# Performance work log

Measured on AMD Instinct MI355X. Metric: run time of the kernel, lower is better.

Reference implementation:

```python
import jax, jax.numpy as jnp
import numpy as np

N_HEAD, D_MODEL, D_K, D_V = 8, 512, 64, 64
B, S = 4, 2048
LN_EPS = 1e-5


def setup_inputs() -> dict:
    key = jax.random.key(0)
    ks = jax.random.split(key, 12)
    std_qk = np.sqrt(2.0 / (D_MODEL + D_K))
    std_v = np.sqrt(2.0 / (D_MODEL + D_V))
    return {
        "q": jax.random.normal(ks[0], (B, S, D_MODEL), jnp.float32),
        "k": jax.random.normal(ks[1], (B, S, D_MODEL), jnp.float32),
        "v": jax.random.normal(ks[2], (B, S, D_MODEL), jnp.float32),
        "w_qs": jax.random.normal(ks[3], (N_HEAD * D_K, D_MODEL), jnp.float32) * std_qk,
        "b_qs": jnp.zeros((N_HEAD * D_K,), jnp.float32),
        "w_ks": jax.random.normal(ks[4], (N_HEAD * D_K, D_MODEL), jnp.float32) * std_qk,
        "b_ks": jnp.zeros((N_HEAD * D_K,), jnp.float32),
        "w_vs": jax.random.normal(ks[5], (N_HEAD * D_V, D_MODEL), jnp.float32) * std_v,
        "b_vs": jnp.zeros((N_HEAD * D_V,), jnp.float32),
        "w_fc": jax.random.normal(ks[6], (D_MODEL, N_HEAD * D_V), jnp.float32) * np.sqrt(2.0 / (D_MODEL + N_HEAD * D_V)),
        "b_fc": jnp.zeros((D_MODEL,), jnp.float32),
        "ln_g": jnp.ones((D_MODEL,), jnp.float32),
        "ln_b": jnp.zeros((D_MODEL,), jnp.float32),
    }


def reference(q, k, v, w_qs, b_qs, w_ks, b_ks, w_vs, b_vs, w_fc, b_fc, ln_g, ln_b):
    sz_b, len_q, _ = q.shape
    residual = q
    temperature = np.power(D_K, 0.5).astype(np.float32)
    # Projections: [b, s, h*dk] -> [h, b, s, dk]  (matches permute(2,0,1,3))
    qh = (jnp.einsum('bsd,fd->bsf', q, w_qs) + b_qs).reshape(sz_b, len_q, N_HEAD, D_K).transpose(2, 0, 1, 3)
    kh = (jnp.einsum('bsd,fd->bsf', k, w_ks) + b_ks).reshape(sz_b, -1, N_HEAD, D_K).transpose(2, 0, 1, 3)
    vh = (jnp.einsum('bsd,fd->bsf', v, w_vs) + b_vs).reshape(sz_b, -1, N_HEAD, D_V).transpose(2, 0, 1, 3)
    # Scaled dot-product attention (dropout is identity in eval)
    attn = jnp.einsum('hbqd,hbkd->hbqk', qh, kh) / temperature
    attn = jax.nn.softmax(attn, axis=-1)
    out = jnp.einsum('hbqk,hbkv->hbqv', attn, vh)          # [h, b, q, dv]
    out = out.transpose(1, 2, 0, 3).reshape(sz_b, len_q, N_HEAD * D_V)
    out = jnp.einsum('bsf,df->bsd', out, w_fc) + b_fc
    # Residual + LayerNorm
    x = out + residual
    mu = jnp.mean(x, axis=-1, keepdims=True)
    var = jnp.mean(jnp.square(x - mu), axis=-1, keepdims=True)
    x = (x - mu) * jax.lax.rsqrt(var + LN_EPS) * ln_g + ln_b
    # attn returned as [(n_head*b), len_q, len_k] to match torch bmm layout
    return x, attn.reshape(N_HEAD * sz_b, len_q, -1)
```

## Files before the change

kernel.cpp:

```cpp
#include <hip/hip_runtime.h>
#include <hip/hip_bf16.h>

constexpr int NB  = 4;
constexpr int NS  = 2048;
constexpr int NH  = 8;
constexpr int DM  = 512;
constexpr int DKV = 64;
constexpr int HB  = NH * NB;

typedef __attribute__((ext_vector_type(8))) short short8;
typedef __attribute__((ext_vector_type(4))) float f32x4;

__device__ inline unsigned short f2bf(float f) {
    unsigned u = __builtin_bit_cast(unsigned, f);
    u = (u + 0x7fffu + ((u >> 16) & 1u)) >> 16;
    return (unsigned short)u;
}
__device__ inline float bf2f(unsigned short h) {
    unsigned u = ((unsigned)h) << 16;
    return __builtin_bit_cast(float, u);
}
__device__ inline short8 ld8(const unsigned short* p) { return *(const short8*)p; }

__device__ inline short8 pack8(const float* p) {
    f32x4 a = *(const f32x4*)p;
    f32x4 b = *(const f32x4*)(p + 4);
    short8 r;
    r[0] = (short)f2bf(a[0]); r[1] = (short)f2bf(a[1]);
    r[2] = (short)f2bf(a[2]); r[3] = (short)f2bf(a[3]);
    r[4] = (short)f2bf(b[0]); r[5] = (short)f2bf(b[1]);
    r[6] = (short)f2bf(b[2]); r[7] = (short)f2bf(b[3]);
    return r;
}

__device__ inline f32x4 mfma16(short8 a, short8 b, f32x4 c) {
    return __builtin_amdgcn_mfma_f32_16x16x32_bf16(a, b, c, 0, 0, 0);
}

__device__ inline void gl_lds16(const void* g, void* l) {
    __builtin_amdgcn_global_load_lds(
        (const __attribute__((address_space(1))) unsigned*)g,
        (__attribute__((address_space(3))) unsigned*)l, 16, 0, 0);
}

__device__ inline void bar() { __builtin_amdgcn_s_barrier(); }

__global__ __launch_bounds__(256) void k_cvt(const float* __restrict__ x0,
                                             const float* __restrict__ x1,
                                             const float* __restrict__ x2,
                                             const float* __restrict__ w0,
                                             const float* __restrict__ w1,
                                             const float* __restrict__ w2,
                                             const float* __restrict__ w3,
                                             unsigned short* __restrict__ dx0,
                                             unsigned short* __restrict__ dx1,
                                             unsigned short* __restrict__ dx2,
                                             unsigned short* __restrict__ dw0,
                                             unsigned short* __restrict__ dw1,
                                             unsigned short* __restrict__ dw2,
                                             unsigned short* __restrict__ dw3)
{
    const float* s; unsigned short* d; size_t i;
    if (blockIdx.y < 3) {
        switch (blockIdx.y) {
            case 0:  s = x0; d = dx0; break;
            case 1:  s = x1; d = dx1; break;
            default: s = x2; d = dx2; break;
        }
        i = ((size_t)blockIdx.x * 256 + threadIdx.x) * 8;
    } else {
        if (blockIdx.x >= 512) return;
        switch (blockIdx.x >> 7) {
            case 0:  s = w0; d = dw0; break;
            case 1:  s = w1; d = dw1; break;
            case 2:  s = w2; d = dw2; break;
            default: s = w3; d = dw3; break;
        }
        i = ((size_t)(blockIdx.x & 127) * 256 + threadIdx.x) * 8;
    }
    *(short8*)(d + i) = pack8(s + i);
}

__global__ __launch_bounds__(256, 4) void k_proj(const unsigned short* __restrict__ X,
                                              const unsigned short* __restrict__ W,
                                              const float* __restrict__ bias,
                                              unsigned short* __restrict__ out,
                                              float scale, int vtrans)
{
    const int tid = threadIdx.x;
    const int l = tid & 63, w = tid >> 6;
    const int c = l & 15, g = l >> 4;
    const int m0 = blockIdx.y * 64 + w * 16;
    const int f0 = blockIdx.x * 64;
    const int arow = m0 + c;

    f32x4 acc[4] = {};
    const unsigned short* aB = X + (size_t)arow * DM;
    for (int kb = 0; kb < DM; kb += 32) {
        short8 af = ld8(aB + kb + g * 8);
#pragma unroll
        for (int n = 0; n < 4; ++n) {
            short8 bf = ld8(W + (size_t)(f0 + n * 16 + c) * DM + kb + g * 8);
            acc[n] = mfma16(af, bf, acc[n]);
        }
    }
#pragma unroll
    for (int n = 0; n < 4; ++n) {
        const int f = f0 + n * 16 + c;
        const int h = f >> 6, d = f & 63;
        const float bv = bias[f];
#pragma unroll
        for (int r = 0; r < 4; ++r) {
            const int m = m0 + g * 4 + r;
            const int bb = m >> 11, s = m & (NS - 1);
            const int hb = h * NB + bb;
            const float v = (acc[n][r] + bv) * scale;
            const size_t idx = vtrans ? ((size_t)(hb * DKV + d) * NS + s)
                                      : ((size_t)(hb * NS + s) * DKV + d);
            out[idx] = f2bf(v);
        }
    }
}

__global__ __launch_bounds__(256, 4) void k_attn(const unsigned short* __restrict__ Qh,
                                                 const unsigned short* __restrict__ Kh,
                                                 const unsigned short* __restrict__ Vt,
                                                 float* __restrict__ attn,
                                                 unsigned short* __restrict__ Obuf)
{
    __shared__ __align__(16) char kld[2][8192];
    __shared__ __align__(16) char vld[2][8192];
    __shared__ __align__(16) char plds[4 * 2048];
    const int tid = threadIdx.x;
    const int l = tid & 63, w = tid >> 6;
    const int c = l & 15, g = l >> 4;
    constexpr int NT = NS / 64;

    const int bid = blockIdx.x;
    const int wid = (bid & 7) * 128 + (bid >> 3);
    const int hb = wid >> 5;
    const int q0 = (wid & 31) * 64 + w * 16;
    char* myp = plds + w * 2048;

    const char* kbytes = (const char*)(Kh + (size_t)hb * NS * DKV);
    const char* vbytes = (const char*)(Vt + (size_t)hb * DKV * NS);

    const unsigned short* qb = Qh + ((size_t)hb * NS + q0 + c) * DKV + g * 8;
    const short8 qf0 = ld8(qb), qf1 = ld8(qb + 32);

    int koff[2], voff[2];
#pragma unroll
    for (int j = 0; j < 2; ++j) {
        const int D = (w * 2 + j) * 1024 + l * 16;
        const int row = D >> 7;
        const int scolb = (D & 127) ^ ((row & 7) << 4);
        koff[j] = row * 128 + scolb;
        voff[j] = row * (NS * 2) + scolb;
    }
    const int swc = (c & 7) << 4;

    const int ldsbase = w * 2048;

    float ls[4] = {0.f, 0.f, 0.f, 0.f};
    {
        gl_lds16(kbytes + koff[0], kld[0] + ldsbase);
        gl_lds16(kbytes + koff[1], kld[0] + ldsbase + 1024);
        asm volatile("s_waitcnt vmcnt(0)" ::: "memory");
        bar();
        __builtin_amdgcn_sched_barrier(0);
        int cur = 0;
        for (int kt = 0; kt < NT; ++kt) {
            if (kt + 1 < NT) {
                const size_t nb = (size_t)(kt + 1) * 64 * 128;
                gl_lds16(kbytes + nb + koff[0], kld[cur ^ 1] + ldsbase);
                gl_lds16(kbytes + nb + koff[1], kld[cur ^ 1] + ldsbase + 1024);
            }
            if (kt > 0) {
                if (kt + 1 < NT) { asm volatile("s_waitcnt vmcnt(2)" ::: "memory"); }
                else             { asm volatile("s_waitcnt vmcnt(0)" ::: "memory"); }
                bar();
                __builtin_amdgcn_sched_barrier(0);
            }
#pragma unroll
            for (int t = 0; t < 4; ++t) {
                const int rb = (t * 16 + c) * 128;
                const short8 b0 = *(const short8*)(kld[cur] + rb + ((g * 16) ^ swc));
                const short8 b1 = *(const short8*)(kld[cur] + rb + ((64 + g * 16) ^ swc));
                f32x4 z = {};
                z = mfma16(qf0, b0, z);
                z = mfma16(qf1, b1, z);
#pragma unroll
                for (int r = 0; r < 4; ++r) ls[r] += exp2f(z[r]);
            }
            bar();
            cur ^= 1;
        }
    }
    float li[4];
#pragma unroll
    for (int r = 0; r < 4; ++r) {
        float s = ls[r];
        s += __shfl_xor(s, 1);
        s += __shfl_xor(s, 2);
        s += __shfl_xor(s, 4);
        s += __shfl_xor(s, 8);
        li[r] = 1.0f / s;
    }

    f32x4 oacc[4] = {};
    const int srow = l >> 2, sseg = l & 3;
    float* srowp = attn + (size_t)hb * NS * NS + (size_t)(q0 + srow) * NS + sseg * 16;
    const int swsr = (srow & 7) << 4;

    {
        gl_lds16(kbytes + koff[0], kld[0] + ldsbase);
        gl_lds16(kbytes + koff[1], kld[0] + ldsbase + 1024);
        gl_lds16(vbytes + voff[0], vld[0] + ldsbase);
        gl_lds16(vbytes + voff[1], vld[0] + ldsbase + 1024);
        asm volatile("s_waitcnt vmcnt(0)" ::: "memory");
        bar();
        __builtin_amdgcn_sched_barrier(0);
        int cur = 0;
        for (int kt = 0; kt < NT; ++kt) {
            const int k0 = kt * 64;
            if (kt + 1 < NT) {
                const size_t nkb = (size_t)(k0 + 64) * 128;
                const size_t nvb = (size_t)(k0 + 64) * 2;
                gl_lds16(kbytes + nkb + koff[0], kld[cur ^ 1] + ldsbase);
                gl_lds16(kbytes + nkb + koff[1], kld[cur ^ 1] + ldsbase + 1024);
                gl_lds16(vbytes + nvb + voff[0], vld[cur ^ 1] + ldsbase);
                gl_lds16(vbytes + nvb + voff[1], vld[cur ^ 1] + ldsbase + 1024);
            }
            if (kt > 0) {
                if (kt + 1 < NT) { asm volatile("s_waitcnt vmcnt(8)" ::: "memory"); }
                else             { asm volatile("s_waitcnt vmcnt(4)" ::: "memory"); }
                bar();
                __builtin_amdgcn_sched_barrier(0);
            }
            f32x4 sc[4];
#pragma unroll
            for (int t = 0; t < 4; ++t) {
                const int rb = (t * 16 + c) * 128;
                const short8 b0 = *(const short8*)(kld[cur] + rb + ((g * 16) ^ swc));
                const short8 b1 = *(const short8*)(kld[cur] + rb + ((64 + g * 16) ^ swc));
                f32x4 z = {};
                z = mfma16(qf0, b0, z);
                z = mfma16(qf1, b1, z);
                sc[t] = z;
            }
#pragma unroll
            for (int t = 0; t < 4; ++t)
#pragma unroll
                for (int r = 0; r < 4; ++r) {
                    const float p = exp2f(sc[t][r]) * li[r];
                    const int row = g * 4 + r;
                    int by = row * 128 + (t * 16 + c) * 2;
                    by ^= (row & 7) << 4;
                    *(unsigned short*)(myp + by) = f2bf(p);
                }
            asm volatile("s_waitcnt lgkmcnt(0)" ::: "memory");
            __builtin_amdgcn_sched_barrier(0);
            {
                const short8 p0 = *(const short8*)(myp + srow * 128 + ((sseg * 32) ^ swsr));
                const short8 p1 = *(const short8*)(myp + srow * 128 + ((sseg * 32 + 16) ^ swsr));
                f32x4 o0, o1, o2, o3;
#pragma unroll
                for (int j = 0; j < 4; ++j) {
                    o0[j] = bf2f((unsigned short)p0[j]);
                    o1[j] = bf2f((unsigned short)p0[4 + j]);
                    o2[j] = bf2f((unsigned short)p1[j]);
                    o3[j] = bf2f((unsigned short)p1[4 + j]);
                }
                float* dst = srowp + k0;
                *(f32x4*)(dst)      = o0;
                *(f32x4*)(dst + 4)  = o1;
                *(f32x4*)(dst + 8)  = o2;
                *(f32x4*)(dst + 12) = o3;
            }
#pragma unroll
            for (int kk = 0; kk < 2; ++kk) {
                const short8 pa = *(const short8*)(myp + c * 128 + ((kk * 64 + g * 16) ^ swc));
#pragma unroll
                for (int n = 0; n < 4; ++n) {
                    const int rb = (n * 16 + c) * 128;
                    const short8 vb = *(const short8*)(vld[cur] + rb + ((kk * 64 + g * 16) ^ swc));
                    oacc[n] = mfma16(pa, vb, oacc[n]);
                }
            }
            bar();
            cur ^= 1;
        }
    }

    const int h = hb >> 2, bb = hb & 3;
#pragma unroll
    for (int n = 0; n < 4; ++n)
#pragma unroll
        for (int r = 0; r < 4; ++r) {
            const int q = q0 + g * 4 + r;
            const int dv = n * 16 + c;
            Obuf[((size_t)(bb * NS + q)) * DM + h * DKV + dv] = f2bf(oacc[n][r]);
        }
}

__global__ __launch_bounds__(256, 4) void k_fc(const unsigned short* __restrict__ O,
                                            const unsigned short* __restrict__ Wfc,
                                            const float* __restrict__ bfc,
                                            const float* __restrict__ resid,
                                            unsigned short* __restrict__ Y)
{
    const int tid = threadIdx.x;
    const int l = tid & 63, w = tid >> 6;
    const int c = l & 15, g = l >> 4;
    const int m0 = blockIdx.y * 64 + w * 16;
    const int f0 = blockIdx.x * 64;
    const int arow = m0 + c;

    f32x4 acc[4] = {};
    const unsigned short* aB = O + (size_t)arow * DM;
    for (int kb = 0; kb < DM; kb += 32) {
        short8 af = ld8(aB + kb + g * 8);
#pragma unroll
        for (int n = 0; n < 4; ++n) {
            short8 bf = ld8(Wfc + (size_t)(f0 + n * 16 + c) * DM + kb + g * 8);
            acc[n] = mfma16(af, bf, acc[n]);
        }
    }
#pragma unroll
    for (int n = 0; n < 4; ++n) {
        const int d = f0 + n * 16 + c;
        const float bv = bfc[d];
#pragma unroll
        for (int r = 0; r < 4; ++r) {
            const int m = m0 + g * 4 + r;
            const float v = acc[n][r] + bv + resid[(size_t)m * DM + d];
            Y[(size_t)m * DM + d] = f2bf(v);
        }
    }
}

__global__ __launch_bounds__(256) void k_ln(const unsigned short* __restrict__ Y,
                                            const float* __restrict__ gam,
                                            const float* __restrict__ bet,
                                            float* __restrict__ out)
{
    const int tid = threadIdx.x;
    const int l = tid & 63, w = tid >> 6;
    const int row = blockIdx.x * 4 + w;

    const short8 yv = ld8(Y + (size_t)row * DM + l * 8);
    float x[8];
#pragma unroll
    for (int j = 0; j < 8; ++j) x[j] = bf2f((unsigned short)yv[j]);

    float s = 0.f;
#pragma unroll
    for (int j = 0; j < 8; ++j) s += x[j];
#pragma unroll
    for (int mask = 1; mask <= 32; mask <<= 1) s += __shfl_xor(s, mask);
    const float mean = s * (1.0f / DM);

    float d2 = 0.f;
#pragma unroll
    for (int j = 0; j < 8; ++j) { const float t = x[j] - mean; d2 += t * t; }
#pragma unroll
    for (int mask = 1; mask <= 32; mask <<= 1) d2 += __shfl_xor(d2, mask);
    const float rstd = rsqrtf(d2 * (1.0f / DM) + 1e-5f);

#pragma unroll
    for (int j = 0; j < 8; ++j) {
        const int d = l * 8 + j;
        out[(size_t)row * DM + d] = (x[j] - mean) * rstd * gam[d] + bet[d];
    }
}

extern "C" void kernel_launch(void* const* d_in, const int* in_sizes, int n_in,
                              void* d_out, int out_size, void* d_ws, size_t ws_size,
                              hipStream_t stream)
{
    const float* q    = (const float*)d_in[0];
    const float* k    = (const float*)d_in[1];
    const float* v    = (const float*)d_in[2];
    const float* w_qs = (const float*)d_in[3];
    const float* b_qs = (const float*)d_in[4];
    const float* w_ks = (const float*)d_in[5];
    const float* b_ks = (const float*)d_in[6];
    const float* w_vs = (const float*)d_in[7];
    const float* b_vs = (const float*)d_in[8];
    const float* w_fc = (const float*)d_in[9];
    const float* b_fc = (const float*)d_in[10];
    const float* ln_g = (const float*)d_in[11];
    const float* ln_b = (const float*)d_in[12];

    char* ws = (char*)d_ws;
    unsigned short* Qh = (unsigned short*)(ws);
    unsigned short* Kh = (unsigned short*)(ws + (8u  << 20));
    unsigned short* Vt = (unsigned short*)(ws + (16u << 20));
    unsigned short* Ob = (unsigned short*)(ws + (24u << 20));
    unsigned short* Yb = (unsigned short*)(ws + (32u << 20));
    unsigned short* Wq = (unsigned short*)(ws + (40u << 20));
    unsigned short* Wk = Wq + (size_t)DM * DM;
    unsigned short* Wv = Wk + (size_t)DM * DM;
    unsigned short* Wf = Wv + (size_t)DM * DM;
    unsigned short* Xq = (unsigned short*)(ws + (48u << 20));
    unsigned short* Xk = (unsigned short*)(ws + (56u << 20));
    unsigned short* Xv = (unsigned short*)(ws + (64u << 20));

    float* xout = (float*)d_out;
    float* attn = xout + (size_t)NB * NS * DM;

    k_cvt<<<dim3(2048, 4), 256, 0, stream>>>(q, k, v, w_qs, w_ks, w_vs, w_fc,
                                             Xq, Xk, Xv, Wq, Wk, Wv, Wf);

    const float qscale = 0.125f * 1.44269504088896340736f;
    const dim3 gproj(8, 128);
    k_proj<<<gproj, 256, 0, stream>>>(Xq, Wq, b_qs, Qh, qscale, 0);
    k_proj<<<gproj, 256, 0, stream>>>(Xk, Wk, b_ks, Kh, 1.0f, 0);
    k_proj<<<gproj, 256, 0, stream>>>(Xv, Wv, b_vs, Vt, 1.0f, 1);

    k_attn<<<1024, 256, 0, stream>>>(Qh, Kh, Vt, attn, Ob);

    k_fc<<<gproj, 256, 0, stream>>>(Ob, Wf, b_fc, q, Yb);
    k_ln<<<NB * NS / 4, 256, 0, stream>>>(Yb, ln_g, ln_b, xout);
}
```

Measured before the change: 428.3 us.

## Split attention row-sum pass into separate kernel, drop LDS staging, merge projections

Merges the three Q/K/V projection launches into one 3D-grid launch. The softmax denominator pass now runs in its own kernel, split over two key halves, so twice as many blocks share the first pass. The main attention kernel reads the two partial sums. Both attention kernels now load K and V fragments straight from global memory into registers instead of double-buffered LDS staging with barriers. This cuts barriers and LDS traffic but relies on cache for reuse across waves, and it adds an extra launch and more redundant global loads.

```diff
diff --git a/kernel.cpp b/kernel.cpp
--- a/kernel.cpp
+++ b/kernel.cpp
@@ -36,14 +36,6 @@
 __device__ inline f32x4 mfma16(short8 a, short8 b, f32x4 c) {
     return __builtin_amdgcn_mfma_f32_16x16x32_bf16(a, b, c, 0, 0, 0);
 }
-
-__device__ inline void gl_lds16(const void* g, void* l) {
-    __builtin_amdgcn_global_load_lds(
-        (const __attribute__((address_space(1))) unsigned*)g,
-        (__attribute__((address_space(3))) unsigned*)l, 16, 0, 0);
-}
-
-__device__ inline void bar() { __builtin_amdgcn_s_barrier(); }
 
 __global__ __launch_bounds__(256) void k_cvt(const float* __restrict__ x0,
                                              const float* __restrict__ x1,
@@ -81,12 +73,27 @@
     *(short8*)(d + i) = pack8(s + i);
 }
 
-__global__ __launch_bounds__(256, 4) void k_proj(const unsigned short* __restrict__ X,
-                                              const unsigned short* __restrict__ W,
-                                              const float* __restrict__ bias,
-                                              unsigned short* __restrict__ out,
-                                              float scale, int vtrans)
-{
+__global__ __launch_bounds__(256, 4) void k_proj3(const unsigned short* __restrict__ Xq,
+                                                  const unsigned short* __restrict__ Xk,
+                                                  const unsigned short* __restrict__ Xv,
+                                                  const unsigned short* __restrict__ Wq,
+                                                  const unsigned short* __restrict__ Wk,
+                                                  const unsigned short* __restrict__ Wv,
+                                                  const float* __restrict__ bq,
+                                                  const float* __restrict__ bk,
+                                                  const float* __restrict__ bv,
+                                                  unsigned short* __restrict__ oq,
+                                                  unsigned short* __restrict__ ok,
+                                                  unsigned short* __restrict__ ov)
+{
+    const unsigned short *X, *W; const float* bias; unsigned short* out;
+    float scale = 1.0f; int vtrans = 0;
+    switch (blockIdx.z) {
+        case 0:  X = Xq; W = Wq; bias = bq; out = oq;
+                 scale = 0.125f * 1.44269504088896340736f; break;
+        case 1:  X = Xk; W = Wk; bias = bk; out = ok; break;
+        default: X = Xv; W = Wv; bias = bv; out = ov; vtrans = 1; break;
+    }
     const int tid = threadIdx.x;
     const int l = tid & 63, w = tid >> 6;
     const int c = l & 15, g = l >> 4;
@@ -108,13 +115,13 @@
     for (int n = 0; n < 4; ++n) {
         const int f = f0 + n * 16 + c;
         const int h = f >> 6, d = f & 63;
-        const float bv = bias[f];
+        const float bvv = bias[f];
 #pragma unroll
         for (int r = 0; r < 4; ++r) {
             const int m = m0 + g * 4 + r;
             const int bb = m >> 11, s = m & (NS - 1);
             const int hb = h * NB + bb;
-            const float v = (acc[n][r] + bv) * scale;
+            const float v = (acc[n][r] + bvv) * scale;
             const size_t idx = vtrans ? ((size_t)(hb * DKV + d) * NS + s)
                                       : ((size_t)(hb * NS + s) * DKV + d);
             out[idx] = f2bf(v);
@@ -122,81 +129,43 @@
     }
 }
 
-__global__ __launch_bounds__(256, 4) void k_attn(const unsigned short* __restrict__ Qh,
-                                                 const unsigned short* __restrict__ Kh,
-                                                 const unsigned short* __restrict__ Vt,
-                                                 float* __restrict__ attn,
-                                                 unsigned short* __restrict__ Obuf)
-{
-    __shared__ __align__(16) char kld[2][8192];
-    __shared__ __align__(16) char vld[2][8192];
-    __shared__ __align__(16) char plds[4 * 2048];
+__global__ __launch_bounds__(256, 4) void k_sum(const unsigned short* __restrict__ Qh,
+                                                const unsigned short* __restrict__ Kh,
+                                                float* __restrict__ Lp)
+{
     const int tid = threadIdx.x;
     const int l = tid & 63, w = tid >> 6;
     const int c = l & 15, g = l >> 4;
-    constexpr int NT = NS / 64;
 
     const int bid = blockIdx.x;
-    const int wid = (bid & 7) * 128 + (bid >> 3);
-    const int hb = wid >> 5;
-    const int q0 = (wid & 31) * 64 + w * 16;
-    char* myp = plds + w * 2048;
-
-    const char* kbytes = (const char*)(Kh + (size_t)hb * NS * DKV);
-    const char* vbytes = (const char*)(Vt + (size_t)hb * DKV * NS);
+    const int wid = (bid & 7) * 256 + (bid >> 3);
+    const int hb = wid >> 6;
+    const int rem = wid & 63;
+    const int q0 = (rem >> 1) * 64 + w * 16;
+    const int ks = rem & 1;
 
     const unsigned short* qb = Qh + ((size_t)hb * NS + q0 + c) * DKV + g * 8;
     const short8 qf0 = ld8(qb), qf1 = ld8(qb + 32);
-
-    int koff[2], voff[2];
-#pragma unroll
-    for (int j = 0; j < 2; ++j) {
-        const int D = (w * 2 + j) * 1024 + l * 16;
-        const int row = D >> 7;
-        const int scolb = (D & 127) ^ ((row & 7) << 4);
-        koff[j] = row * 128 + scolb;
-        voff[j] = row * (NS * 2) + scolb;
-    }
-    const int swc = (c & 7) << 4;
-
-    const int ldsbase = w * 2048;
+    const unsigned short* kslice = Kh + (size_t)hb * NS * DKV + (size_t)ks * 1024 * DKV;
 
     float ls[4] = {0.f, 0.f, 0.f, 0.f};
-    {
-        gl_lds16(kbytes + koff[0], kld[0] + ldsbase);
-        gl_lds16(kbytes + koff[1], kld[0] + ldsbase + 1024);
-        asm volatile("s_waitcnt vmcnt(0)" ::: "memory");
-        bar();
-        __builtin_amdgcn_sched_barrier(0);
-        int cur = 0;
-        for (int kt = 0; kt < NT; ++kt) {
-            if (kt + 1 < NT) {
-                const size_t nb = (size_t)(kt + 1) * 64 * 128;
-                gl_lds16(kbytes + nb + koff[0], kld[cur ^ 1] + ldsbase);
-                gl_lds16(kbytes + nb + koff[1], kld[cur ^ 1] + ldsbase + 1024);
-            }
-            if (kt > 0) {
-                if (kt + 1 < NT) { asm volatile("s_waitcnt vmcnt(2)" ::: "memory"); }
-                else             { asm volatile("s_waitcnt vmcnt(0)" ::: "memory"); }
-                bar();
-                __builtin_amdgcn_sched_barrier(0);
-            }
-#pragma unroll
-            for (int t = 0; t < 4; ++t) {
-                const int rb = (t * 16 + c) * 128;
-                const short8 b0 = *(const short8*)(kld[cur] + rb + ((g * 16) ^ swc));
-                const short8 b1 = *(const short8*)(kld[cur] + rb + ((64 + g * 16) ^ swc));
-                f32x4 z = {};
-                z = mfma16(qf0, b0, z);
-                z = mfma16(qf1, b1, z);
-#pragma unroll
-                for (int r = 0; r < 4; ++r) ls[r] += exp2f(z[r]);
-            }
-            bar();
-            cur ^= 1;
-        }
-    }
-    float li[4];
+    for (int kt = 0; kt < 16; ++kt) {
+        const int k0 = kt * 64;
+        short8 kf[4][2];
+#pragma unroll
+        for (int t = 0; t < 4; ++t) {
+            const unsigned short* kp = kslice + (size_t)(k0 + t * 16 + c) * DKV + g * 8;
+            kf[t][0] = ld8(kp); kf[t][1] = ld8(kp + 32);
+        }
+#pragma unroll
+        for (int t = 0; t < 4; ++t) {
+            f32x4 z = {};
+            z = mfma16(qf0, kf[t][0], z);
+            z = mfma16(qf1, kf[t][1], z);
+#pragma unroll
+            for (int r = 0; r < 4; ++r) ls[r] += exp2f(z[r]);
+        }
+    }
 #pragma unroll
     for (int r = 0; r < 4; ++r) {
         float s = ls[r];
@@ -204,91 +173,104 @@
         s += __shfl_xor(s, 2);
         s += __shfl_xor(s, 4);
         s += __shfl_xor(s, 8);
-        li[r] = 1.0f / s;
+        if (c == 0) Lp[(size_t)ks * HB * NS + hb * NS + q0 + g * 4 + r] = s;
+    }
+}
+
+__global__ __launch_bounds__(256, 4) void k_att(const unsigned short* __restrict__ Qh,
+                                                const unsigned short* __restrict__ Kh,
+                                                const unsigned short* __restrict__ Vt,
+                                                const float* __restrict__ Lp,
+                                                float* __restrict__ attn,
+                                                unsigned short* __restrict__ Obuf)
+{
+    __shared__ __align__(16) char plds[4 * 2048];
+    const int tid = threadIdx.x;
+    const int l = tid & 63, w = tid >> 6;
+    const int c = l & 15, g = l >> 4;
+    constexpr int NT = NS / 64;
+
+    const int bid = blockIdx.x;
+    const int wid = (bid & 7) * 128 + (bid >> 3);
+    const int hb = wid >> 5;
+    const int q0 = (wid & 31) * 64 + w * 16;
+    char* myp = plds + w * 2048;
+
+    const unsigned short* kslice = Kh + (size_t)hb * NS * DKV;
+    const unsigned short* vslice = Vt + (size_t)hb * DKV * NS;
+
+    const unsigned short* qb = Qh + ((size_t)hb * NS + q0 + c) * DKV + g * 8;
+    const short8 qf0 = ld8(qb), qf1 = ld8(qb + 32);
+
+    float li[4];
+#pragma unroll
+    for (int r = 0; r < 4; ++r) {
+        const size_t idx = (size_t)hb * NS + q0 + g * 4 + r;
+        li[r] = 1.0f / (Lp[idx] + Lp[(size_t)HB * NS + idx]);
     }
 
     f32x4 oacc[4] = {};
     const int srow = l >> 2, sseg = l & 3;
     float* srowp = attn + (size_t)hb * NS * NS + (size_t)(q0 + srow) * NS + sseg * 16;
     const int swsr = (srow & 7) << 4;
-
-    {
-        gl_lds16(kbytes + koff[0], kld[0] + ldsbase);
-        gl_lds16(kbytes + koff[1], kld[0] + ldsbase + 1024);
-        gl_lds16(vbytes + voff[0], vld[0] + ldsbase);
-        gl_lds16(vbytes + voff[1], vld[0] + ldsbase + 1024);
-        asm volatile("s_waitcnt vmcnt(0)" ::: "memory");
-        bar();
+    const int swc = (c & 7) << 4;
+
+    for (int kt = 0; kt < NT; ++kt) {
+        const int k0 = kt * 64;
+        short8 kf[4][2], vf[2][4];
+#pragma unroll
+        for (int t = 0; t < 4; ++t) {
+            const unsigned short* kp = kslice + (size_t)(k0 + t * 16 + c) * DKV + g * 8;
+            kf[t][0] = ld8(kp); kf[t][1] = ld8(kp + 32);
+        }
+#pragma unroll
+        for (int kk = 0; kk < 2; ++kk)
+#pragma unroll
+            for (int n = 0; n < 4; ++n)
+                vf[kk][n] = ld8(vslice + (size_t)(n * 16 + c) * NS + k0 + kk * 32 + g * 8);
+        f32x4 sc[4];
+#pragma unroll
+        for (int t = 0; t < 4; ++t) {
+            f32x4 z = {};
+            z = mfma16(qf0, kf[t][0], z);
+            z = mfma16(qf1, kf[t][1], z);
+            sc[t] = z;
+        }
+#pragma unroll
+        for (int t = 0; t < 4; ++t)
+#pragma unroll
+            for (int r = 0; r < 4; ++r) {
+                const float p = exp2f(sc[t][r]) * li[r];
+                const int row = g * 4 + r;
+                int by = row * 128 + (t * 16 + c) * 2;
+                by ^= (row & 7) << 4;
+                *(unsigned short*)(myp + by) = f2bf(p);
+            }
+        asm volatile("s_waitcnt lgkmcnt(0)" ::: "memory");
         __builtin_amdgcn_sched_barrier(0);
-        int cur = 0;
-        for (int kt = 0; kt < NT; ++kt) {
-            const int k0 = kt * 64;
-            if (kt + 1 < NT) {
-                const size_t nkb = (size_t)(k0 + 64) * 128;
-                const size_t nvb = (size_t)(k0 + 64) * 2;
-                gl_lds16(kbytes + nkb + koff[0], kld[cur ^ 1] + ldsbase);
-                gl_lds16(kbytes + nkb + koff[1], kld[cur ^ 1] + ldsbase + 1024);
-                gl_lds16(vbytes + nvb + voff[0], vld[cur ^ 1] + ldsbase);
-                gl_lds16(vbytes + nvb + voff[1], vld[cur ^ 1] + ldsbase + 1024);
+        {
+            const short8 p0 = *(const short8*)(myp + srow * 128 + ((sseg * 32) ^ swsr));
+            const short8 p1 = *(const short8*)(myp + srow * 128 + ((sseg * 32 + 16) ^ swsr));
+            f32x4 o0, o1, o2, o3;
+#pragma unroll
+            for (int j = 0; j < 4; ++j) {
+                o0[j] = bf2f((unsigned short)p0[j]);
+                o1[j] = bf2f((unsigned short)p0[4 + j]);
+                o2[j] = bf2f((unsigned short)p1[j]);
+                o3[j] = bf2f((unsigned short)p1[4 + j]);
             }
-            if (kt > 0) {
-                if (kt + 1 < NT) { asm volatile("s_waitcnt vmcnt(8)" ::: "memory"); }
-                else             { asm volatile("s_waitcnt vmcnt(4)" ::: "memory"); }
-                bar();
-                __builtin_amdgcn_sched_barrier(0);
-            }
-            f32x4 sc[4];
-#pragma unroll
-            for (int t = 0; t < 4; ++t) {
-                const int rb = (t * 16 + c) * 128;
-                const short8 b0 = *(const short8*)(kld[cur] + rb + ((g * 16) ^ swc));
-                const short8 b1 = *(const short8*)(kld[cur] + rb + ((64 + g * 16) ^ swc));
-                f32x4 z = {};
-                z = mfma16(qf0, b0, z);
-                z = mfma16(qf1, b1, z);
-                sc[t] = z;
-            }
-#pragma unroll
-            for (int t = 0; t < 4; ++t)
-#pragma unroll
-                for (int r = 0; r < 4; ++r) {
-                    const float p = exp2f(sc[t][r]) * li[r];
-                    const int row = g * 4 + r;
-                    int by = row * 128 + (t * 16 + c) * 2;
-                    by ^= (row & 7) << 4;
-                    *(unsigned short*)(myp + by) = f2bf(p);
-                }
-            asm volatile("s_waitcnt lgkmcnt(0)" ::: "memory");
-            __builtin_amdgcn_sched_barrier(0);
-            {
-                const short8 p0 = *(const short8*)(myp + srow * 128 + ((sseg * 32) ^ swsr));
-                const short8 p1 = *(const short8*)(myp + srow * 128 + ((sseg * 32 + 16) ^ swsr));
-                f32x4 o0, o1, o2, o3;
-#pragma unroll
-                for (int j = 0; j < 4; ++j) {
-                    o0[j] = bf2f((unsigned short)p0[j]);
-                    o1[j] = bf2f((unsigned short)p0[4 + j]);
-                    o2[j] = bf2f((unsigned short)p1[j]);
-                    o3[j] = bf2f((unsigned short)p1[4 + j]);
-                }
-                float* dst = srowp + k0;
-                *(f32x4*)(dst)      = o0;
-                *(f32x4*)(dst + 4)  = o1;
-                *(f32x4*)(dst + 8)  = o2;
-                *(f32x4*)(dst + 12) = o3;
-            }
-#pragma unroll
-            for (int kk = 0; kk < 2; ++kk) {
-                const short8 pa = *(const short8*)(myp + c * 128 + ((kk * 64 + g * 16) ^ swc));
-#pragma unroll
-                for (int n = 0; n < 4; ++n) {
-                    const int rb = (n * 16 + c) * 128;
-                    const short8 vb = *(const short8*)(vld[cur] + rb + ((kk * 64 + g * 16) ^ swc));
-                    oacc[n] = mfma16(pa, vb, oacc[n]);
-                }
-            }
-            bar();
-            cur ^= 1;
+            float* dst = srowp + k0;
+            *(f32x4*)(dst)      = o0;
+            *(f32x4*)(dst + 4)  = o1;
+            *(f32x4*)(dst + 8)  = o2;
+            *(f32x4*)(dst + 12) = o3;
+        }
+#pragma unroll
+        for (int kk = 0; kk < 2; ++kk) {
+            const short8 pa = *(const short8*)(myp + c * 128 + ((kk * 64 + g * 16) ^ swc));
+#pragma unroll
+            for (int n = 0; n < 4; ++n)
+                oacc[n] = mfma16(pa, vf[kk][n], oacc[n]);
         }
     }
 
@@ -405,6 +387,7 @@
     unsigned short* Xq = (unsigned short*)(ws + (48u << 20));
     unsigned short* Xk = (unsigned short*)(ws + (56u << 20));
     unsigned short* Xv = (unsigned short*)(ws + (64u << 20));
+    float*          Lpart = (float*)(ws + (72u << 20));
 
     float* xout = (float*)d_out;
     float* attn = xout + (size_t)NB * NS * DM;
@@ -412,14 +395,12 @@
     k_cvt<<<dim3(2048, 4), 256, 0, stream>>>(q, k, v, w_qs, w_ks, w_vs, w_fc,
                                              Xq, Xk, Xv, Wq, Wk, Wv, Wf);
 
-    const float qscale = 0.125f * 1.44269504088896340736f;
-    const dim3 gproj(8, 128);
-    k_proj<<<gproj, 256, 0, stream>>>(Xq, Wq, b_qs, Qh, qscale, 0);
-    k_proj<<<gproj, 256, 0, stream>>>(Xk, Wk, b_ks, Kh, 1.0f, 0);
-    k_proj<<<gproj, 256, 0, stream>>>(Xv, Wv, b_vs, Vt, 1.0f, 1);
-
-    k_attn<<<1024, 256, 0, stream>>>(Qh, Kh, Vt, attn, Ob);
-
-    k_fc<<<gproj, 256, 0, stream>>>(Ob, Wf, b_fc, q, Yb);
+    k_proj3<<<dim3(8, 128, 3), 256, 0, stream>>>(Xq, Xk, Xv, Wq, Wk, Wv,
+                                                 b_qs, b_ks, b_vs, Qh, Kh, Vt);
+
+    k_sum<<<2048, 256, 0, stream>>>(Qh, Kh, Lpart);
+    k_att<<<1024, 256, 0, stream>>>(Qh, Kh, Vt, Lpart, attn, Ob);
+
+    k_fc<<<dim3(8, 128), 256, 0, stream>>>(Ob, Wf, b_fc, q, Yb);
     k_ln<<<NB * NS / 4, 256, 0, stream>>>(Yb, ln_g, ln_b, xout);
 }
```

Measured after the change: 623.4 us. 1.46x slower.
